# Performance work log

Measured on AMD Instinct MI355X. Metric: run time of the kernel, lower is better.

The kernel has to match this reference:

```python
import jax, jax.numpy as jnp
from jax import lax
import numpy as np

# db4 (Daubechies-4) filters, matching pywt.Wavelet('db4')
L = 8
_REC_LO = np.array([0.23037781330885523, 0.7148465705525415, 0.6308807679295904,
                    -0.02798376941698385, -0.18703481171888114, 0.030841381835986965,
                    0.032883011666982945, -0.010597401784997278], dtype=np.float32)
_DEC_LO = _REC_LO[::-1].copy()
_DEC_HI = (((-1.0) ** (np.arange(L) + 1)) * _REC_LO).astype(np.float32)  # QMF
_REC_HI = _DEC_HI[::-1].copy()
# lax.conv performs correlation, so use reversed filters to get true convolution.
# rev(dec_lo)=rec_lo, rev(dec_hi)=rec_hi and vice versa.
DEC_K = jnp.asarray(np.stack([_DEC_LO[::-1], _DEC_HI[::-1]])[:, None, :])  # (2,1,L)
REC_K = jnp.asarray(np.stack([_REC_LO[::-1], _REC_HI[::-1]])[None, :, :])  # (1,2,L)

ENHANCE_FACTOR = 1.5
DENOISE_THRESHOLD = 0.2


def _dwt_last(x):
    # pywt single-level DWT (mode='symmetric') along last axis.
    # Equivalent to: conv(sym_pad(x, L-1), dec_filter)[valid][1::2]
    xe = jnp.pad(x, ((0, 0), (L - 1, L - 1)), mode='symmetric')[:, 1:]
    y = lax.conv_general_dilated(xe[:, None, :], DEC_K, (2,), 'VALID',
                                 dimension_numbers=('NCH', 'OIH', 'NCH'))
    return y[:, 0], y[:, 1]  # lo, hi, each (M, (S+L-1)//2)


def _idwt_last(lo, hi):
    # pywt single-level IDWT: upsample (lhs_dilation=2), filter, trim L-2 each side.
    c = jnp.stack([lo, hi], axis=1)  # (M, 2, n)
    y = lax.conv_general_dilated(c, REC_K, (1,), [(1, 1)], lhs_dilation=(2,),
                                 dimension_numbers=('NCH', 'OIH', 'NCH'))
    return y[:, 0]  # (M, 2n - L + 2)


def _dwt2(x):
    # x: (N, H, W) -> aa (cA), da (cH), ad (cV), dd (cD)
    N, H, W = x.shape
    lo, hi = _dwt_last(x.reshape(N * H, W))
    Wc = lo.shape[-1]
    lo = lo.reshape(N, H, Wc)
    hi = hi.reshape(N, H, Wc)

    def colwise(a):
        at = a.transpose(0, 2, 1).reshape(N * Wc, H)
        l, h = _dwt_last(at)
        Hc = l.shape[-1]
        return (l.reshape(N, Wc, Hc).transpose(0, 2, 1),
                h.reshape(N, Wc, Hc).transpose(0, 2, 1))

    aa, da = colwise(lo)
    ad, dd = colwise(hi)
    return aa, da, ad, dd


def _idwt2(aa, da, ad, dd):
    N, Hc, Wc = aa.shape

    def colinv(a, d):
        at = a.transpose(0, 2, 1).reshape(N * Wc, Hc)
        dt = d.transpose(0, 2, 1).reshape(N * Wc, Hc)
        r = _idwt_last(at, dt)
        H = r.shape[-1]
        return r.reshape(N, Wc, H).transpose(0, 2, 1)

    lo = colinv(aa, da)
    hi = colinv(ad, dd)
    H = lo.shape[1]
    out = _idwt_last(lo.reshape(N * H, Wc), hi.reshape(N * H, Wc))
    return out.reshape(N, H, -1)


def _soft_enhance(d):
    # enhance then pywt.threshold(..., mode='soft') with per-(image,channel,band) max
    d = d * ENHANCE_FACTOR
    t = DENOISE_THRESHOLD * jnp.max(jnp.abs(d), axis=(-2, -1), keepdims=True)
    return jnp.sign(d) * jnp.maximum(jnp.abs(d) - t, 0.0)


def setup_inputs() -> dict:
    key = jax.random.key(0)
    x = jax.random.normal(key, (32, 3, 510, 510), dtype=jnp.float32)
    return {'x': x}


def reference(x):
    B, C, H, W = x.shape
    z = x.reshape(B * C, H, W)
    a1, h1, v1, d1 = _dwt2(z)
    a2, h2, v2, d2 = _dwt2(a1)
    h2s, v2s, d2s = _soft_enhance(h2), _soft_enhance(v2), _soft_enhance(d2)
    h1s, v1s, d1s = _soft_enhance(h1), _soft_enhance(v1), _soft_enhance(d1)
    a1r = _idwt2(a2, h2s, v2s, d2s)
    out = _idwt2(a1r, h1s, v1s, d1s)
    return out.reshape(B, C, H, W)
```

## Files before the change

### kernel.cpp

```cpp
#include <hip/hip_runtime.h>

__device__ constexpr float DEC_LO[8] = {
    -0.010597401784997278f, 0.032883011666982945f, 0.030841381835986965f,
    -0.18703481171888114f, -0.02798376941698385f, 0.6308807679295904f,
    0.7148465705525415f, 0.23037781330885523f};
__device__ constexpr float DEC_HI[8] = {
    -0.23037781330885523f, 0.7148465705525415f, -0.6308807679295904f,
    -0.02798376941698385f, 0.18703481171888114f, 0.030841381835986965f,
    -0.032883011666982945f, -0.010597401784997278f};
__device__ constexpr float REC_LO[8] = {
    0.23037781330885523f, 0.7148465705525415f, 0.6308807679295904f,
    -0.02798376941698385f, -0.18703481171888114f, 0.030841381835986965f,
    0.032883011666982945f, -0.010597401784997278f};
__device__ constexpr float REC_HI[8] = {
    -0.010597401784997278f, -0.032883011666982945f, 0.030841381835986965f,
    0.18703481171888114f, -0.02798376941698385f, -0.6308807679295904f,
    0.7148465705525415f, -0.23037781330885523f};

__device__ __forceinline__ float soft_enh(float v, float th) {
    float e = 1.5f * v;
    float a = fabsf(e) - th;
    return a > 0.0f ? copysignf(a, e) : 0.0f;
}

#define TB 32
#define TO 64

__global__ __launch_bounds__(256, 4) void fused_dwt2_k(
    const float* __restrict__ x, int S, int Nc, int tiles,
    float* __restrict__ aa, float* __restrict__ da,
    float* __restrict__ ad, float* __restrict__ dd,
    unsigned* __restrict__ mx_da, unsigned* __restrict__ mx_ad,
    unsigned* __restrict__ mx_dd)
{
    int b = blockIdx.x;
    int tx = b % tiles, ty = (b / tiles) % tiles, m = b / (tiles * tiles);
    int jh0 = ty * TB, jw0 = tx * TB;
    int r0 = 2 * jh0 - 6, c0 = 2 * jw0 - 6;
    const float* xm = x + (size_t)m * S * S;

    __shared__ float RB[70][68];

    int tid = threadIdx.x;
    bool colv = (c0 >= 0) && (c0 + 71 < S);

    int e0 = tid, e1 = tid + 256, e2 = tid + 512;
    bool has2 = (e2 < 560);

    auto prow = [&](int e) -> const float* {
        int pr = r0 + (e >> 3);
        pr = pr < 0 ? -1 - pr : pr;
        pr = pr >= S ? 2 * S - 1 - pr : pr;
        return xm + (size_t)pr * S;
    };

    float f0[16], f1[16], f2[16];
    if (colv) {
        const float* s0 = prow(e0) + (c0 + 8 * (e0 & 7));
        const float* s1 = prow(e1) + (c0 + 8 * (e1 & 7));
#pragma unroll
        for (int i = 0; i < 8; ++i) {
            float2 v = *reinterpret_cast<const float2*>(s0 + 2 * i);
            f0[2 * i] = v.x; f0[2 * i + 1] = v.y;
        }
#pragma unroll
        for (int i = 0; i < 8; ++i) {
            float2 v = *reinterpret_cast<const float2*>(s1 + 2 * i);
            f1[2 * i] = v.x; f1[2 * i + 1] = v.y;
        }
        if (has2) {
            const float* s2 = prow(e2) + (c0 + 8 * (e2 & 7));
#pragma unroll
            for (int i = 0; i < 8; ++i) {
                float2 v = *reinterpret_cast<const float2*>(s2 + 2 * i);
                f2[2 * i] = v.x; f2[2 * i + 1] = v.y;
            }
        }
    } else {
        auto gath = [&](int e, float* f) {
            const float* row = prow(e);
            int base = c0 + 8 * (e & 7);
#pragma unroll
            for (int i = 0; i < 16; ++i) {
                int p = base + i;
                p = p < 0 ? -1 - p : p;
                p = p >= S ? 2 * S - 1 - p : p;
                f[i] = row[p];
            }
        };
        gath(e0, f0);
        gath(e1, f1);
        if (has2) gath(e2, f2);
    }

    auto rdwt = [&](int e, const float* f) {
        float lo[4], hi[4];
#pragma unroll
        for (int i = 0; i < 4; ++i) {
            float alo = 0.f, ahi = 0.f;
#pragma unroll
            for (int t = 0; t < 8; ++t) {
                float v = f[2 * i + 7 - t];
                alo = fmaf(DEC_LO[t], v, alo);
                ahi = fmaf(DEC_HI[t], v, ahi);
            }
            lo[i] = alo; hi[i] = ahi;
        }
        int r = e >> 3, c4 = 4 * (e & 7);
        *reinterpret_cast<float4*>(&RB[r][c4]) = make_float4(lo[0], lo[1], lo[2], lo[3]);
        *reinterpret_cast<float4*>(&RB[r][32 + c4]) = make_float4(hi[0], hi[1], hi[2], hi[3]);
    };
    rdwt(e0, f0);
    rdwt(e1, f1);
    if (has2) rdwt(e2, f2);
    __syncthreads();

    int jj = tid & 31, g = tid >> 5;
    int jw = jw0 + jj;
    float mh = 0.f, mv = 0.f, md = 0.f;
#pragma unroll
    for (int pass = 0; pass < 2; ++pass) {
        int rbase = 8 * g + 4 * pass;
        float L[10], H[10];
#pragma unroll
        for (int rr = 0; rr < 10; ++rr) {
            L[rr] = RB[rbase + rr][jj];
            H[rr] = RB[rbase + rr][32 + jj];
        }
#pragma unroll
        for (int k = 0; k < 2; ++k) {
            float vaa = 0.f, vda = 0.f, vad = 0.f, vdd = 0.f;
#pragma unroll
            for (int t = 0; t < 8; ++t) {
                float l = L[2 * k + 7 - t];
                float h = H[2 * k + 7 - t];
                vaa = fmaf(DEC_LO[t], l, vaa);
                vda = fmaf(DEC_HI[t], l, vda);
                vad = fmaf(DEC_LO[t], h, vad);
                vdd = fmaf(DEC_HI[t], h, vdd);
            }
            int jh = jh0 + 4 * g + 2 * pass + k;
            if (jh < Nc && jw < Nc) {
                size_t o = ((size_t)m * Nc + jh) * Nc + jw;
                aa[o] = vaa; da[o] = vda; ad[o] = vad; dd[o] = vdd;
                mh = fmaxf(mh, fabsf(vda));
                mv = fmaxf(mv, fabsf(vad));
                md = fmaxf(md, fabsf(vdd));
            }
        }
    }
#pragma unroll
    for (int off = 32; off; off >>= 1) {
        mh = fmaxf(mh, __shfl_down(mh, off));
        mv = fmaxf(mv, __shfl_down(mv, off));
        md = fmaxf(md, __shfl_down(md, off));
    }
    __shared__ float sm[3][4];
    int wv = tid >> 6, ln = tid & 63;
    if (ln == 0) { sm[0][wv] = mh; sm[1][wv] = mv; sm[2][wv] = md; }
    __syncthreads();
    if (tid == 0) {
        float A = fmaxf(fmaxf(sm[0][0], sm[0][1]), fmaxf(sm[0][2], sm[0][3]));
        float B = fmaxf(fmaxf(sm[1][0], sm[1][1]), fmaxf(sm[1][2], sm[1][3]));
        float C = fmaxf(fmaxf(sm[2][0], sm[2][1]), fmaxf(sm[2][2], sm[2][3]));
        atomicMax(mx_da + m, __float_as_uint(A));
        atomicMax(mx_ad + m, __float_as_uint(B));
        atomicMax(mx_dd + m, __float_as_uint(C));
    }
}

__global__ __launch_bounds__(256, 4) void fused_idwt2_k(
    const float* __restrict__ a, const float* __restrict__ h,
    const float* __restrict__ v, const float* __restrict__ d,
    const unsigned* __restrict__ mxh, const unsigned* __restrict__ mxv,
    const unsigned* __restrict__ mxd,
    int n, int Ho, int tiles, float* __restrict__ out)
{
    int b = blockIdx.x;
    int tx = b % tiles, ty = (b / tiles) % tiles, m = b / (tiles * tiles);
    int i0 = ty * TO, u0 = tx * TO;
    int jr0 = i0 >> 1, jc0 = u0 >> 1;

    __shared__ float LH[TO][71];

    int tid = threadIdx.x;
    float th_h = 0.2f * (1.5f * __uint_as_float(mxh[m]));
    float th_v = 0.2f * (1.5f * __uint_as_float(mxv[m]));
    float th_d = 0.2f * (1.5f * __uint_as_float(mxd[m]));
    const float* am = a + (size_t)m * n * n;
    const float* hm = h + (size_t)m * n * n;
    const float* vm = v + (size_t)m * n * n;
    const float* dm = d + (size_t)m * n * n;

    auto coltask = [&](int task) {
        int g = task / 35, jc = task % 35;
        int jcg = jc0 + jc; if (jcg > n - 1) jcg = n - 1;
        float Ar[7], Hr[7], Vr[7], Dr[7];
#pragma unroll
        for (int rr = 0; rr < 7; ++rr) {
            int jr = jr0 + 4 * g + rr; if (jr > n - 1) jr = n - 1;
            size_t o = (size_t)jr * n + jcg;
            Ar[rr] = am[o];
            Hr[rr] = hm[o];
            Vr[rr] = vm[o];
            Dr[rr] = dm[o];
        }
#pragma unroll
        for (int rr = 0; rr < 7; ++rr) {
            Hr[rr] = soft_enh(Hr[rr], th_h);
            Vr[rr] = soft_enh(Vr[rr], th_v);
            Dr[rr] = soft_enh(Dr[rr], th_d);
        }
#pragma unroll
        for (int pass = 0; pass < 2; ++pass) {
            int P = 2 * g + pass;
            float acc_lo[4], acc_hi[4];
#pragma unroll
            for (int k = 0; k < 4; ++k) { acc_lo[k] = 0.f; acc_hi[k] = 0.f; }
#pragma unroll
            for (int rl = 0; rl < 5; ++rl) {
                int rr = 2 * pass + rl;
                float av = Ar[rr], hv = Hr[rr], vv = Vr[rr], dv = Dr[rr];
#pragma unroll
                for (int t = 0; t < 8; ++t) {
                    int k = 2 * rl + t - 6;
                    if (k >= 0 && k < 4) {
                        acc_lo[k] = fmaf(REC_LO[t], av, fmaf(REC_HI[t], hv, acc_lo[k]));
                        acc_hi[k] = fmaf(REC_LO[t], vv, fmaf(REC_HI[t], dv, acc_hi[k]));
                    }
                }
            }
#pragma unroll
            for (int k = 0; k < 4; ++k) {
                LH[4 * P + k][jc] = acc_lo[k];
                LH[4 * P + k][35 + jc] = acc_hi[k];
            }
        }
    };
    coltask(tid);
    if (tid + 256 < 8 * 35) coltask(tid + 256);
    __syncthreads();

    for (int e = tid; e < TO * TO; e += 256) {
        int il = e >> 6, ul = e & 63;
        int t0 = ul & 1;
        float acc = 0.f;
#pragma unroll
        for (int s = 0; s < 4; ++s) {
            int t = t0 + 2 * s;
            int c = (ul + 6 - t) >> 1;
            acc = fmaf(REC_LO[t], LH[il][c], acc);
            acc = fmaf(REC_HI[t], LH[il][35 + c], acc);
        }
        int gi = i0 + il, gu = u0 + ul;
        if (gi < Ho && gu < Ho)
            out[((size_t)m * Ho + gi) * Ho + gu] = acc;
    }
}

extern "C" void kernel_launch(void* const* d_in, const int* in_sizes, int n_in,
                              void* d_out, int out_size, void* d_ws, size_t ws_size,
                              hipStream_t stream) {
    const float* x = (const float*)d_in[0];
    float* out = (float*)d_out;
    float* ws = (float*)d_ws;

    const int M = 96, S1 = 510, N1 = 258, N2 = 132;
    const long S_l1 = (long)M * N1 * N1;
    const long S_l2 = (long)M * N2 * N2;

    float* aa1 = ws;
    float* h1  = aa1 + S_l1;
    float* v1  = h1 + S_l1;
    float* d1  = v1 + S_l1;
    float* a1r = d1 + S_l1;
    float* a2  = a1r + S_l1;
    float* h2  = a2 + S_l2;
    float* v2  = h2 + S_l2;
    float* d2  = v2 + S_l2;
    unsigned* th = (unsigned*)(d2 + S_l2);

    long need = 5 * S_l1 + 4 * S_l2 + 576;
    if (ws_size < (size_t)need * sizeof(float)) return;

    unsigned *th_h1 = th, *th_v1 = th + 96, *th_d1 = th + 192;
    unsigned *th_h2 = th + 288, *th_v2 = th + 384, *th_d2 = th + 480;

    hipMemsetAsync(th, 0, 576 * sizeof(unsigned), stream);

    fused_dwt2_k<<<9 * 9 * M, 256, 0, stream>>>(x, S1, N1, 9, aa1, h1, v1, d1,
                                                th_h1, th_v1, th_d1);
    fused_dwt2_k<<<5 * 5 * M, 256, 0, stream>>>(aa1, N1, N2, 5, a2, h2, v2, d2,
                                                th_h2, th_v2, th_d2);
    fused_idwt2_k<<<5 * 5 * M, 256, 0, stream>>>(a2, h2, v2, d2, th_h2, th_v2, th_d2,
                                                 N2, N1, 5, a1r);
    fused_idwt2_k<<<8 * 8 * M, 256, 0, stream>>>(a1r, h1, v1, d1, th_h1, th_v1, th_d1,
                                                 N1, S1, 8, out);
}
```

Baseline: 337.1 us.

## Stage raw input tile in LDS via direct global-to-LDS loads in forward DWT

The forward DWT kernel now copies the 70x70 input halo tile (row stride 76) into shared memory with __builtin_amdgcn_global_load_lds, doing symmetric-edge clamping per element, then reads float4 vectors from LDS for the row filter. This replaces per-thread float2 and scalar gathers into registers and the separate boundary path. It is meant to coalesce global reads and cut register pressure. The cost is an extra ~21KB of LDS per block, which may lower occupancy, plus an extra sync and per-element index math.

```diff
diff --git a/kernel.cpp b/kernel.cpp
--- a/kernel.cpp
+++ b/kernel.cpp
@@ -26,6 +26,9 @@
 #define TB 32
 #define TO 64
 
+#define RAW_STRIDE 76
+#define RAW_CHUNKS 84
+
 __global__ __launch_bounds__(256, 4) void fused_dwt2_k(
     const float* __restrict__ x, int S, int Nc, int tiles,
     float* __restrict__ aa, float* __restrict__ da,
@@ -39,61 +42,49 @@
     int r0 = 2 * jh0 - 6, c0 = 2 * jw0 - 6;
     const float* xm = x + (size_t)m * S * S;
 
+    __shared__ float raw[RAW_CHUNKS * 64];
     __shared__ float RB[70][68];
 
     int tid = threadIdx.x;
-    bool colv = (c0 >= 0) && (c0 + 71 < S);
-
-    int e0 = tid, e1 = tid + 256, e2 = tid + 512;
-    bool has2 = (e2 < 560);
-
-    auto prow = [&](int e) -> const float* {
-        int pr = r0 + (e >> 3);
+    int wv = tid >> 6, ln = tid & 63;
+
+    for (int j = 0; j < RAW_CHUNKS / 4; ++j) {
+        int w = wv * (RAW_CHUNKS / 4) + j;
+        unsigned idx = (unsigned)(64 * w + ln);
+        if (idx > 5319u) idx = 5319u;
+        unsigned r = idx / RAW_STRIDE;
+        unsigned c = idx - r * RAW_STRIDE;
+        if (c > 69u) c = 69u;
+        int pr = r0 + (int)r;
         pr = pr < 0 ? -1 - pr : pr;
         pr = pr >= S ? 2 * S - 1 - pr : pr;
-        return xm + (size_t)pr * S;
-    };
-
-    float f0[16], f1[16], f2[16];
-    if (colv) {
-        const float* s0 = prow(e0) + (c0 + 8 * (e0 & 7));
-        const float* s1 = prow(e1) + (c0 + 8 * (e1 & 7));
-#pragma unroll
-        for (int i = 0; i < 8; ++i) {
-            float2 v = *reinterpret_cast<const float2*>(s0 + 2 * i);
-            f0[2 * i] = v.x; f0[2 * i + 1] = v.y;
-        }
-#pragma unroll
-        for (int i = 0; i < 8; ++i) {
-            float2 v = *reinterpret_cast<const float2*>(s1 + 2 * i);
-            f1[2 * i] = v.x; f1[2 * i + 1] = v.y;
-        }
-        if (has2) {
-            const float* s2 = prow(e2) + (c0 + 8 * (e2 & 7));
-#pragma unroll
-            for (int i = 0; i < 8; ++i) {
-                float2 v = *reinterpret_cast<const float2*>(s2 + 2 * i);
-                f2[2 * i] = v.x; f2[2 * i + 1] = v.y;
-            }
-        }
-    } else {
-        auto gath = [&](int e, float* f) {
-            const float* row = prow(e);
-            int base = c0 + 8 * (e & 7);
-#pragma unroll
-            for (int i = 0; i < 16; ++i) {
-                int p = base + i;
-                p = p < 0 ? -1 - p : p;
-                p = p >= S ? 2 * S - 1 - p : p;
-                f[i] = row[p];
-            }
-        };
-        gath(e0, f0);
-        gath(e1, f1);
-        if (has2) gath(e2, f2);
-    }
-
-    auto rdwt = [&](int e, const float* f) {
+        int pc = c0 + (int)c;
+        pc = pc < 0 ? -1 - pc : pc;
+        pc = pc >= S ? 2 * S - 1 - pc : pc;
+        const float* g = xm + (size_t)pr * S + pc;
+#if defined(__has_builtin) && __has_builtin(__builtin_amdgcn_global_load_lds)
+        __builtin_amdgcn_global_load_lds(
+            (const __attribute__((address_space(1))) void*)g,
+            (__attribute__((address_space(3))) void*)(&raw[64 * w]),
+            4, 0, 0);
+#else
+        raw[64 * w + ln] = *g;
+#endif
+    }
+    __syncthreads();
+
+    for (int e = tid; e < 560; e += 256) {
+        int r = e >> 3, q = e & 7;
+        const float* base = &raw[RAW_STRIDE * r + 8 * q];
+        float f[16];
+        float4 A = *reinterpret_cast<const float4*>(base);
+        float4 B = *reinterpret_cast<const float4*>(base + 4);
+        float4 C = *reinterpret_cast<const float4*>(base + 8);
+        float4 D = *reinterpret_cast<const float4*>(base + 12);
+        f[0] = A.x; f[1] = A.y; f[2] = A.z; f[3] = A.w;
+        f[4] = B.x; f[5] = B.y; f[6] = B.z; f[7] = B.w;
+        f[8] = C.x; f[9] = C.y; f[10] = C.z; f[11] = C.w;
+        f[12] = D.x; f[13] = D.y; f[14] = D.z; f[15] = D.w;
         float lo[4], hi[4];
 #pragma unroll
         for (int i = 0; i < 4; ++i) {
@@ -106,13 +97,10 @@
             }
             lo[i] = alo; hi[i] = ahi;
         }
-        int r = e >> 3, c4 = 4 * (e & 7);
+        int c4 = 4 * q;
         *reinterpret_cast<float4*>(&RB[r][c4]) = make_float4(lo[0], lo[1], lo[2], lo[3]);
         *reinterpret_cast<float4*>(&RB[r][32 + c4]) = make_float4(hi[0], hi[1], hi[2], hi[3]);
-    };
-    rdwt(e0, f0);
-    rdwt(e1, f1);
-    if (has2) rdwt(e2, f2);
+    }
     __syncthreads();
 
     int jj = tid & 31, g = tid >> 5;
@@ -156,7 +144,6 @@
         md = fmaxf(md, __shfl_down(md, off));
     }
     __shared__ float sm[3][4];
-    int wv = tid >> 6, ln = tid & 63;
     if (ln == 0) { sm[0][wv] = mh; sm[1][wv] = mv; sm[2][wv] = md; }
     __syncthreads();
     if (tid == 0) {
```

Measured after the change: 335.7 us. No clear change (-0.4%).

## Fuse both inverse DWT levels into one kernel, recomputing level-1 approximation per tile

Applied to the files above, without the earlier changes.

Replaces the two separate inverse-DWT launches with one kernel. For each output tile it reconstructs the needed 35x35 patch of the level-1 approximation from the level-2 coefficients in shared memory, then runs the final inverse transform. This removes the write and re-read of the full a1r intermediate and one kernel launch. In exchange it recomputes overlapping halo regions across tiles, uses more shared memory, and adds synchronisations, which may reduce occupancy.

```diff
diff --git a/kernel.cpp b/kernel.cpp
--- a/kernel.cpp
+++ b/kernel.cpp
@@ -169,58 +169,130 @@
     }
 }
 
-__global__ __launch_bounds__(256, 4) void fused_idwt2_k(
-    const float* __restrict__ a, const float* __restrict__ h,
-    const float* __restrict__ v, const float* __restrict__ d,
-    const unsigned* __restrict__ mxh, const unsigned* __restrict__ mxv,
-    const unsigned* __restrict__ mxd,
-    int n, int Ho, int tiles, float* __restrict__ out)
+__global__ __launch_bounds__(256, 4) void fused_irec_k(
+    const float* __restrict__ a2, const float* __restrict__ h2,
+    const float* __restrict__ v2, const float* __restrict__ d2,
+    const float* __restrict__ h1, const float* __restrict__ v1,
+    const float* __restrict__ d1,
+    const unsigned* __restrict__ mx2h, const unsigned* __restrict__ mx2v,
+    const unsigned* __restrict__ mx2d,
+    const unsigned* __restrict__ mx1h, const unsigned* __restrict__ mx1v,
+    const unsigned* __restrict__ mx1d,
+    int n2, int n1, int Ho, int tiles, float* __restrict__ out)
 {
     int b = blockIdx.x;
     int tx = b % tiles, ty = (b / tiles) % tiles, m = b / (tiles * tiles);
     int i0 = ty * TO, u0 = tx * TO;
     int jr0 = i0 >> 1, jc0 = u0 >> 1;
-
-    __shared__ float LH[TO][71];
+    int q0r = jr0 >> 1, q0c = jc0 >> 1;
+
+    __shared__ float AH[35][44];
+    __shared__ float AR[35][36];
+    __shared__ float LH[64][71];
 
     int tid = threadIdx.x;
-    float th_h = 0.2f * (1.5f * __uint_as_float(mxh[m]));
-    float th_v = 0.2f * (1.5f * __uint_as_float(mxv[m]));
-    float th_d = 0.2f * (1.5f * __uint_as_float(mxd[m]));
-    const float* am = a + (size_t)m * n * n;
-    const float* hm = h + (size_t)m * n * n;
-    const float* vm = v + (size_t)m * n * n;
-    const float* dm = d + (size_t)m * n * n;
-
-    auto coltask = [&](int task) {
-        int g = task / 35, jc = task % 35;
-        int jcg = jc0 + jc; if (jcg > n - 1) jcg = n - 1;
-        float Ar[7], Hr[7], Vr[7], Dr[7];
+    float th2_h = 0.2f * (1.5f * __uint_as_float(mx2h[m]));
+    float th2_v = 0.2f * (1.5f * __uint_as_float(mx2v[m]));
+    float th2_d = 0.2f * (1.5f * __uint_as_float(mx2d[m]));
+    float th1_h = 0.2f * (1.5f * __uint_as_float(mx1h[m]));
+    float th1_v = 0.2f * (1.5f * __uint_as_float(mx1v[m]));
+    float th1_d = 0.2f * (1.5f * __uint_as_float(mx1d[m]));
+    const float* a2m = a2 + (size_t)m * n2 * n2;
+    const float* h2m = h2 + (size_t)m * n2 * n2;
+    const float* v2m = v2 + (size_t)m * n2 * n2;
+    const float* d2m = d2 + (size_t)m * n2 * n2;
+    const float* h1m = h1 + (size_t)m * n1 * n1;
+    const float* v1m = v1 + (size_t)m * n1 * n1;
+    const float* d1m = d1 + (size_t)m * n1 * n1;
+
+    int g2 = tid / 21, cc = tid % 21;
+    bool act1a = (tid < 189);
+    float A2r[5], H2r[5], V2r[5], D2r[5];
+    if (act1a) {
+        int c2 = q0c + cc; if (c2 > n2 - 1) c2 = n2 - 1;
+#pragma unroll
+        for (int rl = 0; rl < 5; ++rl) {
+            int j2 = q0r + 2 * g2 + rl; if (j2 > n2 - 1) j2 = n2 - 1;
+            size_t o = (size_t)j2 * n2 + c2;
+            A2r[rl] = a2m[o]; H2r[rl] = h2m[o];
+            V2r[rl] = v2m[o]; D2r[rl] = d2m[o];
+        }
+    }
+
+    int gA = tid / 35, jcA = tid % 35;
+    int jcg = jc0 + jcA; if (jcg > n1 - 1) jcg = n1 - 1;
+    int baseA = jr0 + 4 * gA;
+    float Hg[7], Vg[7], Dg[7];
+#pragma unroll
+    for (int rr = 0; rr < 7; ++rr) {
+        int jr = baseA + rr; if (jr > n1 - 1) jr = n1 - 1;
+        size_t o = (size_t)jr * n1 + jcg;
+        Hg[rr] = h1m[o]; Vg[rr] = v1m[o]; Dg[rr] = d1m[o];
+    }
+
+    if (act1a) {
+#pragma unroll
+        for (int rl = 0; rl < 5; ++rl) {
+            H2r[rl] = soft_enh(H2r[rl], th2_h);
+            V2r[rl] = soft_enh(V2r[rl], th2_v);
+            D2r[rl] = soft_enh(D2r[rl], th2_d);
+        }
+        float alo[4], ahi[4];
+#pragma unroll
+        for (int k = 0; k < 4; ++k) { alo[k] = 0.f; ahi[k] = 0.f; }
+#pragma unroll
+        for (int rl = 0; rl < 5; ++rl) {
+#pragma unroll
+            for (int t = 0; t < 8; ++t) {
+                int k = 2 * rl + t - 6;
+                if (k >= 0 && k < 4) {
+                    alo[k] = fmaf(REC_LO[t], A2r[rl], fmaf(REC_HI[t], H2r[rl], alo[k]));
+                    ahi[k] = fmaf(REC_LO[t], V2r[rl], fmaf(REC_HI[t], D2r[rl], ahi[k]));
+                }
+            }
+        }
+#pragma unroll
+        for (int k = 0; k < 4; ++k) {
+            int p = 4 * g2 + k;
+            if (p < 35) { AH[p][cc] = alo[k]; AH[p][22 + cc] = ahi[k]; }
+        }
+    }
+    __syncthreads();
+
+    for (int e = tid; e < 1225; e += 256) {
+        int p = e / 35, cl = e % 35;
+        int t0 = cl & 1;
+        float acc = 0.f;
+#pragma unroll
+        for (int s = 0; s < 4; ++s) {
+            int t = t0 + 2 * s;
+            int c = (cl + 6 - t) >> 1;
+            acc = fmaf(REC_LO[t], AH[p][c], acc);
+            acc = fmaf(REC_HI[t], AH[p][22 + c], acc);
+        }
+        AR[p][cl] = acc;
+    }
+    __syncthreads();
+
+    {
+        float Ar[7], Hs[7], Vs[7], Ds[7];
 #pragma unroll
         for (int rr = 0; rr < 7; ++rr) {
-            int jr = jr0 + 4 * g + rr; if (jr > n - 1) jr = n - 1;
-            size_t o = (size_t)jr * n + jcg;
-            Ar[rr] = am[o];
-            Hr[rr] = hm[o];
-            Vr[rr] = vm[o];
-            Dr[rr] = dm[o];
-        }
-#pragma unroll
-        for (int rr = 0; rr < 7; ++rr) {
-            Hr[rr] = soft_enh(Hr[rr], th_h);
-            Vr[rr] = soft_enh(Vr[rr], th_v);
-            Dr[rr] = soft_enh(Dr[rr], th_d);
+            Ar[rr] = AR[4 * gA + rr][jcA];
+            Hs[rr] = soft_enh(Hg[rr], th1_h);
+            Vs[rr] = soft_enh(Vg[rr], th1_v);
+            Ds[rr] = soft_enh(Dg[rr], th1_d);
         }
 #pragma unroll
         for (int pass = 0; pass < 2; ++pass) {
-            int P = 2 * g + pass;
+            int P = 2 * gA + pass;
             float acc_lo[4], acc_hi[4];
 #pragma unroll
             for (int k = 0; k < 4; ++k) { acc_lo[k] = 0.f; acc_hi[k] = 0.f; }
 #pragma unroll
             for (int rl = 0; rl < 5; ++rl) {
                 int rr = 2 * pass + rl;
-                float av = Ar[rr], hv = Hr[rr], vv = Vr[rr], dv = Dr[rr];
+                float av = Ar[rr], hv = Hs[rr], vv = Vs[rr], dv = Ds[rr];
 #pragma unroll
                 for (int t = 0; t < 8; ++t) {
                     int k = 2 * rl + t - 6;
@@ -232,13 +304,52 @@
             }
 #pragma unroll
             for (int k = 0; k < 4; ++k) {
-                LH[4 * P + k][jc] = acc_lo[k];
-                LH[4 * P + k][35 + jc] = acc_hi[k];
-            }
-        }
-    };
-    coltask(tid);
-    if (tid + 256 < 8 * 35) coltask(tid + 256);
+                LH[4 * P + k][jcA] = acc_lo[k];
+                LH[4 * P + k][35 + jcA] = acc_hi[k];
+            }
+        }
+    }
+    if (tid < 24) {
+        int tk = tid + 256;
+        int gB = tk / 35, jcB = tk % 35;
+        int jcgB = jc0 + jcB; if (jcgB > n1 - 1) jcgB = n1 - 1;
+        int baseB = jr0 + 4 * gB;
+        float Ar[7], Hs[7], Vs[7], Ds[7];
+#pragma unroll
+        for (int rr = 0; rr < 7; ++rr) {
+            int jr = baseB + rr; if (jr > n1 - 1) jr = n1 - 1;
+            size_t o = (size_t)jr * n1 + jcgB;
+            Ar[rr] = AR[4 * gB + rr][jcB];
+            Hs[rr] = soft_enh(h1m[o], th1_h);
+            Vs[rr] = soft_enh(v1m[o], th1_v);
+            Ds[rr] = soft_enh(d1m[o], th1_d);
+        }
+#pragma unroll
+        for (int pass = 0; pass < 2; ++pass) {
+            int P = 2 * gB + pass;
+            float acc_lo[4], acc_hi[4];
+#pragma unroll
+            for (int k = 0; k < 4; ++k) { acc_lo[k] = 0.f; acc_hi[k] = 0.f; }
+#pragma unroll
+            for (int rl = 0; rl < 5; ++rl) {
+                int rr = 2 * pass + rl;
+                float av = Ar[rr], hv = Hs[rr], vv = Vs[rr], dv = Ds[rr];
+#pragma unroll
+                for (int t = 0; t < 8; ++t) {
+                    int k = 2 * rl + t - 6;
+                    if (k >= 0 && k < 4) {
+                        acc_lo[k] = fmaf(REC_LO[t], av, fmaf(REC_HI[t], hv, acc_lo[k]));
+                        acc_hi[k] = fmaf(REC_LO[t], vv, fmaf(REC_HI[t], dv, acc_hi[k]));
+                    }
+                }
+            }
+#pragma unroll
+            for (int k = 0; k < 4; ++k) {
+                LH[4 * P + k][jcB] = acc_lo[k];
+                LH[4 * P + k][35 + jcB] = acc_hi[k];
+            }
+        }
+    }
     __syncthreads();
 
     for (int e = tid; e < TO * TO; e += 256) {
@@ -273,14 +384,13 @@
     float* h1  = aa1 + S_l1;
     float* v1  = h1 + S_l1;
     float* d1  = v1 + S_l1;
-    float* a1r = d1 + S_l1;
-    float* a2  = a1r + S_l1;
+    float* a2  = d1 + S_l1;
     float* h2  = a2 + S_l2;
     float* v2  = h2 + S_l2;
     float* d2  = v2 + S_l2;
     unsigned* th = (unsigned*)(d2 + S_l2);
 
-    long need = 5 * S_l1 + 4 * S_l2 + 576;
+    long need = 4 * S_l1 + 4 * S_l2 + 576;
     if (ws_size < (size_t)need * sizeof(float)) return;
 
     unsigned *th_h1 = th, *th_v1 = th + 96, *th_d1 = th + 192;
@@ -292,8 +402,8 @@
                                                 th_h1, th_v1, th_d1);
     fused_dwt2_k<<<5 * 5 * M, 256, 0, stream>>>(aa1, N1, N2, 5, a2, h2, v2, d2,
                                                 th_h2, th_v2, th_d2);
-    fused_idwt2_k<<<5 * 5 * M, 256, 0, stream>>>(a2, h2, v2, d2, th_h2, th_v2, th_d2,
-                                                 N2, N1, 5, a1r);
-    fused_idwt2_k<<<8 * 8 * M, 256, 0, stream>>>(a1r, h1, v1, d1, th_h1, th_v1, th_d1,
-                                                 N1, S1, 8, out);
+    fused_irec_k<<<8 * 8 * M, 256, 0, stream>>>(a2, h2, v2, d2, h1, v1, d1,
+                                                th_h2, th_v2, th_d2,
+                                                th_h1, th_v1, th_d1,
+                                                N2, N1, S1, 8, out);
 }
```

Result: faster. 326.2 us (-3.3%).
